# Performance work log

Measured on AMD Instinct MI355X. Metric: run time of the kernel, lower is better.

## Reference

```python
import jax, jax.numpy as jnp
import numpy as np

B, T, C, H, NT = 1, 1024, 768, 12, 8
D = C // H  # 64
POWER_ITERS = 4
DP_TEMP = 0.8
ESR_GAMMA = 0.02
ESR_ALPHA = 0.1


def rmsnorm(x, w, eps=1e-6):
    rms = jax.lax.rsqrt(jnp.mean(x * x, axis=-1, keepdims=True) + eps)
    return x * rms * w


def setup_inputs():
    key = jax.random.key(0)
    k0, k1, k2 = jax.random.split(key, 3)
    return {
        "x": jax.random.normal(k0, (B, T, C), jnp.float32),
        "W_qkvg": jax.random.normal(k1, (4 * C, C), jnp.float32) * 0.02,
        "W_out": jax.random.normal(k2, (C, C), jnp.float32) * 0.02,
        "lam": jnp.float32(1.5),
        "log_tau": -0.5 * jnp.ones((H, NT), jnp.float32),
        "logit_w": jnp.zeros((H, NT), jnp.float32),
        "beta": 1.5 * jnp.ones((H,), jnp.float32),
        "out_scale": jnp.ones((H,), jnp.float32),
        "dp_scale": jnp.ones((H,), jnp.float32),
        "logk_scale": jnp.ones((H,), jnp.float32),
        "dt_logit": jnp.float32(np.log(1.0 / 1e-8)),  # dt=1.0 -> logit = log(dt/(1-dt+1e-8))
        "g_norm_w": jnp.ones((D,), jnp.float32),
    }


def reference(x, W_qkvg, W_out, lam, log_tau, logit_w, beta, out_scale,
              dp_scale, logk_scale, dt_logit, g_norm_w):
    # qkvg projection and head split
    qkvg = x @ W_qkvg.T                                    # [B,T,4C]
    q, k, v, g = jnp.split(qkvg, 4, axis=-1)
    to_heads = lambda t: t.reshape(B, T, H, D).transpose(0, 2, 1, 3)  # [B,H,T,D]
    q, k, v, g = map(to_heads, (q, k, v, g))
    g = rmsnorm(g, g_norm_w)

    # pairwise squared distance ||g_i - g_j||^2
    g2 = jnp.sum(g * g, axis=-1)                           # [B,H,T]
    s = jnp.maximum(g2[..., :, None] + g2[..., None, :]
                    - 2.0 * jnp.einsum('bhid,bhjd->bhij', g, g), 0.0)  # [B,H,T,T]

    # fractional log-kernel: logsumexp_t[-(beta/2) log1p(s/(4 tau_t)) + log w_t]
    tau = jnp.maximum(jnp.exp(log_tau), 1e-6)              # [H,NT]
    w = jax.nn.softmax(logit_w, axis=-1)                   # [H,NT]
    beta_c = jnp.clip(beta, 0.5, 2.5)                      # [H]
    log_k_per = -(beta_c[None, :, None, None, None] / 2.0) * jnp.log1p(
        s[:, :, None] / (4.0 * tau[None, :, :, None, None]))          # [B,H,NT,T,T]
    logK = jax.nn.logsumexp(log_k_per + jnp.log(w + 1e-12)[None, :, :, None, None], axis=2)
    logK = logK * logk_scale[None, :, None, None]

    # dot-product scores
    dp = jnp.einsum('bhid,bhjd->bhij', q, k) * (dp_scale[None, :, None, None]
                                                / (np.sqrt(D) * DP_TEMP))

    # causal Markov normalize: blend, mask, stable row-softmax
    mask = jnp.tril(jnp.ones((T, T), bool))[None, None]    # [1,1,T,T]
    blended = lam * dp + (1.0 - lam) * logK
    blended = jnp.where(mask, blended, -jnp.inf)
    mx = jnp.max(blended, axis=-1, keepdims=True)
    mx = jnp.where(jnp.isfinite(mx), mx, 0.0)
    Kmat = jnp.exp(jnp.maximum(blended - mx, -60.0)) * mask
    P = Kmat / jnp.maximum(Kmat.sum(-1, keepdims=True), 1e-12)

    # power iteration for left stationary pi with full-support teleport
    pi0 = jnp.full((B, H, 1, T), 1.0 / T, P.dtype)
    def step(pi, _):
        p = (1.0 - ESR_GAMMA) * (pi @ P) + ESR_GAMMA / T
        p = p / jnp.maximum(p.sum(-1, keepdims=True), 1e-12)
        return p, None
    pi, _ = jax.lax.scan(step, pi0, None, length=POWER_ITERS)
    pi = jax.lax.stop_gradient(pi[..., 0, :])              # [B,H,T] (detached)

    # causal approximation to additive reversibilization
    P_adj = (pi[..., None, :] / jnp.maximum(pi[..., :, None], 1e-12)) \
            * jnp.swapaxes(P, -1, -2)                      # P*_ij = (pi_j/pi_i) P_ji
    P_rev = 0.5 * (P + P_adj) * mask
    P_rev = P_rev / jnp.maximum(P_rev.sum(-1, keepdims=True), 1e-12)

    dt = jax.nn.sigmoid(dt_logit)
    alpha = ESR_ALPHA * dt                                  # scale_alpha_by_dt=True
    P_fin = (1.0 - alpha) * P + alpha * P_rev

    y = (P_fin @ v) * out_scale[None, :, None, None]       # [B,H,T,D]
    y = y.transpose(0, 2, 1, 3).reshape(B, T, C)
    return y @ W_out.T
```

## Files before the change

kernel.cpp:

```cpp
#include <hip/hip_runtime.h>
#include <math.h>

#define TSEQ 1024
#define CD   768
#define HN   12
#define DD   64

#define OFF_QKVG   0
#define OFF_QH     3145728
#define OFF_KH     3538944
#define OFF_GH     3932160
#define OFF_VHT    4325376
#define OFF_G2     4718592
#define OFF_YB     4730880
#define OFF_CONSTS 5124096
#define OFF_OPART  5124608
#define OFF_LS     5911040
#define OFF_PD     5923328
#define OFF_XB     5935616
#define OFF_WQB    6328832
#define OFF_WOB    7508480
#define NZERO4     199680

#define N_XB  786432
#define N_WQB 2359296
#define N_WOB 589824

typedef __bf16 bf16x8 __attribute__((ext_vector_type(8)));
typedef float  f32x4  __attribute__((ext_vector_type(4)));
typedef unsigned short u16x8 __attribute__((ext_vector_type(8)));
typedef unsigned short u16x4 __attribute__((ext_vector_type(4)));

__device__ inline unsigned short f2bf(float f) {
  unsigned int u = __float_as_uint(f);
  return (unsigned short)((u + 0x7fffu + ((u >> 16) & 1u)) >> 16);
}


__global__ __launch_bounds__(64) void prep_kernel(
    const float* __restrict__ lam_p, const float* __restrict__ log_tau,
    const float* __restrict__ logit_w, const float* __restrict__ beta,
    const float* __restrict__ out_scale, const float* __restrict__ dp_scale,
    const float* __restrict__ logk_scale, const float* __restrict__ dt_logit,
    float* __restrict__ consts) {
  int h = threadIdx.x;
  if (h == 0) {
    float dt = 1.0f / (1.0f + __expf(-dt_logit[0]));
    consts[288] = 0.1f * dt;
  }
  if (h < HN) {
    float lam = lam_p[0];
    float* c = consts + h * 24;
    c[0] = lam * dp_scale[h] * (1.0f / 6.4f);
    c[1] = (1.0f - lam) * logk_scale[h];
    float b = fminf(fmaxf(beta[h], 0.5f), 2.5f);
    c[2] = 0.5f * b;
    c[3] = out_scale[h];
    float m = -1e30f;
    float lw[8];
    bool uni = true;
    for (int t = 0; t < 8; t++) {
      lw[t] = logit_w[h * 8 + t];
      m = fmaxf(m, lw[t]);
      if (log_tau[h * 8 + t] != log_tau[h * 8] || lw[t] != lw[0]) uni = false;
    }
    float s = 0.f;
    float e[8];
    for (int t = 0; t < 8; t++) { e[t] = __expf(lw[t] - m); s += e[t]; }
    for (int t = 0; t < 8; t++) {
      float w = e[t] / s;
      c[12 + t] = log2f(w + 1e-12f);
      float tau = fmaxf(__expf(log_tau[h * 8 + t]), 1e-6f);
      c[4 + t] = 1.0f / (4.0f * tau);
    }
    c[20] = uni ? 1.0f : 8.0f;
  }
}

__global__ __launch_bounds__(256) void zero_kernel(float4* __restrict__ p, int n4) {
  int i = blockIdx.x * 256 + threadIdx.x;
  for (; i < n4; i += gridDim.x * 256) p[i] = make_float4(0.f, 0.f, 0.f, 0.f);
}

__global__ __launch_bounds__(256) void convert_kernel(
    const float* __restrict__ x, const float* __restrict__ wq,
    const float* __restrict__ wo, unsigned short* __restrict__ xb,
    unsigned short* __restrict__ wqb, unsigned short* __restrict__ wob) {
  int i8 = (blockIdx.x * 256 + threadIdx.x) * 8;
  const float* src;
  unsigned short* dst;
  int off;
  if (i8 < N_XB) { src = x; dst = xb; off = i8; }
  else if (i8 < N_XB + N_WQB) { src = wq; dst = wqb; off = i8 - N_XB; }
  else if (i8 < N_XB + N_WQB + N_WOB) { src = wo; dst = wob; off = i8 - N_XB - N_WQB; }
  else return;
  float4 a = *(const float4*)&src[off];
  float4 b = *(const float4*)&src[off + 4];
  u16x8 u;
  u[0] = f2bf(a.x); u[1] = f2bf(a.y); u[2] = f2bf(a.z); u[3] = f2bf(a.w);
  u[4] = f2bf(b.x); u[5] = f2bf(b.y); u[6] = f2bf(b.z); u[7] = f2bf(b.w);
  *(u16x8*)&dst[off] = u;
}

__global__ __launch_bounds__(256, 2) void gemm_bf16_abT(
    const unsigned short* __restrict__ A, const unsigned short* __restrict__ B,
    float* __restrict__ Cm, int M, int N, int K) {
  __shared__ __align__(16) unsigned short As[128 * 72];
  __shared__ __align__(16) unsigned short Bs[64 * 72];
  int t = threadIdx.x;
  int lane = t & 63, w = t >> 6;
  int quad = lane >> 4, tx = lane & 15;
  int n0 = blockIdx.x * 64, m0 = blockIdx.y * 128;

  f32x4 acc[2][4] = {};
  int r_ = t >> 3, c8 = (t & 7) * 8;

  for (int k0 = 0; k0 < K; k0 += 64) {
    __syncthreads();
#pragma unroll
    for (int rep = 0; rep < 4; rep++) {
      int r = rep * 32 + r_;
      *(u16x8*)&As[r * 72 + c8] = *(const u16x8*)&A[(size_t)(m0 + r) * K + k0 + c8];
    }
#pragma unroll
    for (int rep = 0; rep < 2; rep++) {
      int r = rep * 32 + r_;
      *(u16x8*)&Bs[r * 72 + c8] = *(const u16x8*)&B[(size_t)(n0 + r) * K + k0 + c8];
    }
    __syncthreads();

#pragma unroll
    for (int ks = 0; ks < 2; ks++) {
      bf16x8 af[2];
#pragma unroll
      for (int mi = 0; mi < 2; mi++)
        af[mi] = *(const bf16x8*)&As[(32 * w + mi * 16 + tx) * 72 + ks * 32 + quad * 8];
#pragma unroll
      for (int ni = 0; ni < 4; ni++) {
        bf16x8 bv = *(const bf16x8*)&Bs[(ni * 16 + tx) * 72 + ks * 32 + quad * 8];
#pragma unroll
        for (int mi = 0; mi < 2; mi++)
          acc[mi][ni] = __builtin_amdgcn_mfma_f32_16x16x32_bf16(af[mi], bv, acc[mi][ni], 0, 0, 0);
      }
    }
  }

#pragma unroll
  for (int mi = 0; mi < 2; mi++)
#pragma unroll
    for (int ni = 0; ni < 4; ni++)
#pragma unroll
      for (int reg = 0; reg < 4; reg++) {
        int row = m0 + 32 * w + mi * 16 + quad * 4 + reg;
        Cm[(size_t)row * N + n0 + ni * 16 + tx] = acc[mi][ni][reg];
      }
}

__global__ __launch_bounds__(256) void pack_kernel(
    const float* __restrict__ qkvg, const float* __restrict__ g_norm_w,
    unsigned short* __restrict__ qh, unsigned short* __restrict__ kh,
    unsigned short* __restrict__ gh, unsigned short* __restrict__ vhT,
    float* __restrict__ g2) {
  int h = blockIdx.y;
  int t0 = blockIdx.x * 64;
  int t = threadIdx.x;
  __shared__ float tile[64][65];
  __shared__ float gw[64];
  __shared__ float part[64][4];
  __shared__ float rr[64];
  if (t < 64) gw[t] = g_norm_w[t];

#pragma unroll
  for (int rep = 0; rep < 2; rep++) {
    int idx = rep * 256 + t;
    int r = idx >> 3, c8 = (idx & 7) * 8;
    const float* sq = &qkvg[(size_t)(t0 + r) * 3072 + h * 64 + c8];
    const float* sk = sq + CD;
    u16x8 uq, uk;
#pragma unroll
    for (int j = 0; j < 8; j++) { uq[j] = f2bf(sq[j]); uk[j] = f2bf(sk[j]); }
    *(u16x8*)&qh[(size_t)(h * 1024 + t0 + r) * 64 + c8] = uq;
    *(u16x8*)&kh[(size_t)(h * 1024 + t0 + r) * 64 + c8] = uk;
  }

#pragma unroll 4
  for (int rep = 0; rep < 16; rep++) {
    int idx = rep * 256 + t;
    int r = idx >> 6, d = idx & 63;
    tile[r][d] = qkvg[(size_t)(t0 + r) * 3072 + 3 * CD + h * 64 + d];
  }
  __syncthreads();
  {
    int row = t >> 2, seg = t & 3;
    float s1 = 0.f;
    for (int d = seg * 16; d < seg * 16 + 16; d++) { float g = tile[row][d]; s1 += g * g; }
    part[row][seg] = s1;
  }
  __syncthreads();
  if (t < 64)
    rr[t] = rsqrtf((part[t][0] + part[t][1] + part[t][2] + part[t][3]) * (1.f / 64.f) + 1e-6f);
  __syncthreads();
  {
    int row = t >> 2, seg = t & 3;
    float rv = rr[row];
    float s2 = 0.f;
    u16x8 ua, ub;
#pragma unroll
    for (int j = 0; j < 8; j++) {
      float v = tile[row][seg * 16 + j] * rv * gw[seg * 16 + j];
      unsigned short us = f2bf(v); ua[j] = us;
      float vb = __uint_as_float((unsigned)us << 16); s2 += vb * vb;
    }
#pragma unroll
    for (int j = 0; j < 8; j++) {
      float v = tile[row][seg * 16 + 8 + j] * rv * gw[seg * 16 + 8 + j];
      unsigned short us = f2bf(v); ub[j] = us;
      float vb = __uint_as_float((unsigned)us << 16); s2 += vb * vb;
    }
    *(u16x8*)&gh[(size_t)(h * 1024 + t0 + row) * 64 + seg * 16] = ua;
    *(u16x8*)&gh[(size_t)(h * 1024 + t0 + row) * 64 + seg * 16 + 8] = ub;
    part[row][seg] = s2;
  }
  __syncthreads();
  if (t < 64) g2[h * 1024 + t0 + t] = part[t][0] + part[t][1] + part[t][2] + part[t][3];

  __syncthreads();
#pragma unroll 4
  for (int rep = 0; rep < 16; rep++) {
    int idx = rep * 256 + t;
    int r = idx >> 6, d = idx & 63;
    tile[r][d] = qkvg[(size_t)(t0 + r) * 3072 + 2 * CD + h * 64 + d];
  }
  __syncthreads();
#pragma unroll
  for (int rep = 0; rep < 2; rep++) {
    int idx = rep * 256 + t;
    int d = idx >> 3, tc8 = (idx & 7) * 8;
    u16x8 u;
#pragma unroll
    for (int j = 0; j < 8; j++) u[j] = f2bf(tile[tc8 + j][d]);
    *(u16x8*)&vhT[(size_t)(h * 64 + d) * 1024 + t0 + tc8] = u;
  }
}

__global__ __launch_bounds__(256, 3) void flash_kernel(
    const unsigned short* __restrict__ qh, const unsigned short* __restrict__ kh,
    const unsigned short* __restrict__ gh, const unsigned short* __restrict__ vhT,
    const float* __restrict__ g2, const float* __restrict__ consts,
    float* __restrict__ Opart, float* __restrict__ lsp, float* __restrict__ pdp) {
  int h = blockIdx.y;
  int uu = 143 - (int)blockIdx.x;
  int it = 0, rem = uu;
  for (it = 0; it < 32; ++it) {
    int njt_ = (it >> 1) + 1;
    int nc = (njt_ + 1) >> 1;
    if (rem < nc) break;
    rem -= nc;
  }
  int njt = (it >> 1) + 1;
  int jt0 = rem * 2;
  int jt1 = (jt0 + 2 < njt) ? (jt0 + 2) : njt;
  bool owns_diag = (jt1 == njt);
  int i0 = it * 32;
  int t = threadIdx.x;
  int lane = t & 63, w = t >> 6;
  int quad = lane >> 4, tx = lane & 15;
  int mi = w >> 1, nb = (w & 1) * 2;

  __shared__ __align__(16) unsigned short Qa[32 * 72];
  __shared__ __align__(16) unsigned short Ga[32 * 72];
  __shared__ __align__(16) unsigned short Ks[64 * 72];
  __shared__ __align__(16) unsigned short Gjs[64 * 72];
  __shared__ __align__(16) unsigned short Vt[64 * 72];
  __shared__ __align__(16) unsigned short psh[32 * 72];
  __shared__ float g2i[32], g2j[64], pdiag[32];

  const float* ch = consts + h * 24;
  float dpc2 = ch[0] * 1.44269504089f;
  float lkc = ch[1], bh2 = ch[2];
  int ntt = (int)ch[20];
  float i4t0 = ch[4];
  float inv4tau[8], logw[8];
#pragma unroll
  for (int tt = 0; tt < 8; tt++) { inv4tau[tt] = ch[4 + tt]; logw[tt] = ch[12 + tt]; }

  {
    int r = t >> 3, c8 = (t & 7) * 8;
    *(u16x8*)&Qa[r * 72 + c8] = *(const u16x8*)&qh[(size_t)(h * 1024 + i0 + r) * 64 + c8];
    *(u16x8*)&Ga[r * 72 + c8] = *(const u16x8*)&gh[(size_t)(h * 1024 + i0 + r) * 64 + c8];
  }
  if (t < 32) { g2i[t] = g2[h * 1024 + i0 + t]; pdiag[t] = 0.f; }
  __syncthreads();

  bf16x8 aq[2], ag[2];
#pragma unroll
  for (int ks = 0; ks < 2; ks++) {
    aq[ks] = *(const bf16x8*)&Qa[(mi * 16 + tx) * 72 + ks * 32 + quad * 8];
    ag[ks] = *(const bf16x8*)&Ga[(mi * 16 + tx) * 72 + ks * 32 + quad * 8];
  }

  f32x4 Oc[2] = {};
  float rowacc[4] = {0.f, 0.f, 0.f, 0.f};

  for (int jt = jt0; jt < jt1; jt++) {
    int j0 = jt * 64;
    __syncthreads();
    {
      int r4 = t >> 2, cb = (t & 3) * 16;
      const unsigned short* kp = &kh[(size_t)(h * 1024 + j0 + r4) * 64 + cb];
      const unsigned short* gp = &gh[(size_t)(h * 1024 + j0 + r4) * 64 + cb];
      const unsigned short* vp = &vhT[(size_t)(h * 64 + r4) * 1024 + j0 + cb];
      *(u16x8*)&Ks[r4 * 72 + cb] = *(const u16x8*)kp;
      *(u16x8*)&Ks[r4 * 72 + cb + 8] = *(const u16x8*)(kp + 8);
      *(u16x8*)&Gjs[r4 * 72 + cb] = *(const u16x8*)gp;
      *(u16x8*)&Gjs[r4 * 72 + cb + 8] = *(const u16x8*)(gp + 8);
      *(u16x8*)&Vt[r4 * 72 + cb] = *(const u16x8*)vp;
      *(u16x8*)&Vt[r4 * 72 + cb + 8] = *(const u16x8*)(vp + 8);
    }
    if (t < 64) g2j[t] = g2[h * 1024 + j0 + t];
    __syncthreads();

    f32x4 sqk[2] = {}, sgg[2] = {};
#pragma unroll
    for (int ni2 = 0; ni2 < 2; ni2++) {
#pragma unroll
      for (int ks = 0; ks < 2; ks++) {
        bf16x8 bk = *(const bf16x8*)&Ks[((nb + ni2) * 16 + tx) * 72 + ks * 32 + quad * 8];
        sqk[ni2] = __builtin_amdgcn_mfma_f32_16x16x32_bf16(aq[ks], bk, sqk[ni2], 0, 0, 0);
        bf16x8 bg = *(const bf16x8*)&Gjs[((nb + ni2) * 16 + tx) * 72 + ks * 32 + quad * 8];
        sgg[ni2] = __builtin_amdgcn_mfma_f32_16x16x32_bf16(ag[ks], bg, sgg[ni2], 0, 0, 0);
      }
    }

    float rs[4] = {0.f, 0.f, 0.f, 0.f};
#pragma unroll
    for (int ni2 = 0; ni2 < 2; ni2++) {
      int colg = j0 + (nb + ni2) * 16 + tx;
      float g2jv = g2j[(nb + ni2) * 16 + tx];
#pragma unroll
      for (int reg = 0; reg < 4; reg++) {
        int rowl = mi * 16 + quad * 4 + reg;
        int gi = i0 + rowl;
        float s = fmaxf(g2i[rowl] + g2jv - 2.0f * sgg[ni2][reg], 0.0f);
        float lse2;
        if (ntt == 1) {
          lse2 = -bh2 * __builtin_amdgcn_logf(fmaf(s, i4t0, 1.0f));
        } else {
          float se = 0.f;
#pragma unroll
          for (int tt = 0; tt < 8; tt++) {
            float lv = __builtin_amdgcn_logf(fmaf(s, inv4tau[tt], 1.0f));
            se += __builtin_amdgcn_exp2f(fmaf(-bh2, lv, logw[tt]));
          }
          lse2 = __builtin_amdgcn_logf(se + 1e-30f);
        }
        float b = fmaf(dpc2, sqk[ni2][reg], lkc * lse2);
        float p = (colg <= gi) ? __builtin_amdgcn_exp2f(b) : 0.0f;
        rs[reg] += p;
        psh[rowl * 72 + (nb + ni2) * 16 + tx] = f2bf(p);
        if (colg == gi) pdiag[rowl] = p;
      }
    }
#pragma unroll
    for (int reg = 0; reg < 4; reg++) {
#pragma unroll
      for (int m = 1; m < 16; m <<= 1) rs[reg] += __shfl_xor(rs[reg], m, 64);
      rowacc[reg] += rs[reg];
    }
    __syncthreads();

    bf16x8 ap[2];
#pragma unroll
    for (int ks = 0; ks < 2; ks++)
      ap[ks] = *(const bf16x8*)&psh[(mi * 16 + tx) * 72 + ks * 32 + quad * 8];
#pragma unroll
    for (int nd2 = 0; nd2 < 2; nd2++) {
#pragma unroll
      for (int ks = 0; ks < 2; ks++) {
        bf16x8 bv = *(const bf16x8*)&Vt[((nb + nd2) * 16 + tx) * 72 + ks * 32 + quad * 8];
        Oc[nd2] = __builtin_amdgcn_mfma_f32_16x16x32_bf16(ap[ks], bv, Oc[nd2], 0, 0, 0);
      }
    }
  }
  __syncthreads();

#pragma unroll
  for (int nd2 = 0; nd2 < 2; nd2++) {
#pragma unroll
    for (int reg = 0; reg < 4; reg++) {
      int row = i0 + mi * 16 + quad * 4 + reg;
      atomicAdd(&Opart[(size_t)(h * 1024 + row) * 64 + (nb + nd2) * 16 + tx], Oc[nd2][reg]);
    }
  }
  if (tx == 0) {
#pragma unroll
    for (int reg = 0; reg < 4; reg++)
      atomicAdd(&lsp[h * 1024 + i0 + mi * 16 + quad * 4 + reg], rowacc[reg]);
  }
  if (owns_diag && t < 32) pdp[h * 1024 + i0 + t] = pdiag[t];
}

__global__ __launch_bounds__(256) void finalize_kernel(
    const float* __restrict__ Opart, const float* __restrict__ lsp,
    const float* __restrict__ pdp, const float* __restrict__ qkvg,
    const float* __restrict__ consts, unsigned short* __restrict__ yb) {
  int h = blockIdx.y;
  int t = threadIdx.x;
  int rl = t >> 4, d4 = t & 15;
  int gi = blockIdx.x * 16 + rl;
  float alpha = consts[288];
  float osc = consts[h * 24 + 3];
  float l = fmaxf(lsp[h * TSEQ + gi], 1e-12f);
  float Pii = pdp[h * TSEQ + gi] / l;
  float inv1p = 1.0f / (1.0f + Pii);
  float c1 = (1.0f - alpha) + alpha * inv1p;
  float c2 = alpha * Pii * inv1p;
  float invl = 1.0f / l;
  float4 Ov = *(const float4*)&Opart[(size_t)(h * 1024 + gi) * 64 + 4 * d4];
  float4 vi = *(const float4*)&qkvg[(size_t)gi * 3072 + 2 * CD + h * 64 + 4 * d4];
  u16x4 o;
  o[0] = f2bf(osc * (c1 * Ov.x * invl + c2 * vi.x));
  o[1] = f2bf(osc * (c1 * Ov.y * invl + c2 * vi.y));
  o[2] = f2bf(osc * (c1 * Ov.z * invl + c2 * vi.z));
  o[3] = f2bf(osc * (c1 * Ov.w * invl + c2 * vi.w));
  *(u16x4*)&yb[(size_t)gi * CD + h * 64 + 4 * d4] = o;
}

extern "C" void kernel_launch(void* const* d_in, const int* in_sizes, int n_in,
                              void* d_out, int out_size, void* d_ws, size_t ws_size,
                              hipStream_t stream) {
  (void)in_sizes; (void)n_in; (void)out_size; (void)ws_size;
  const float* x          = (const float*)d_in[0];
  const float* W_qkvg     = (const float*)d_in[1];
  const float* W_out      = (const float*)d_in[2];
  const float* lam        = (const float*)d_in[3];
  const float* log_tau    = (const float*)d_in[4];
  const float* logit_w    = (const float*)d_in[5];
  const float* beta       = (const float*)d_in[6];
  const float* out_scale  = (const float*)d_in[7];
  const float* dp_scale   = (const float*)d_in[8];
  const float* logk_scale = (const float*)d_in[9];
  const float* dt_logit   = (const float*)d_in[10];
  const float* g_norm_w   = (const float*)d_in[11];
  float* ws = (float*)d_ws;
  float* qkvg   = ws + OFF_QKVG;
  unsigned short* qh  = (unsigned short*)(ws + OFF_QH);
  unsigned short* kh  = (unsigned short*)(ws + OFF_KH);
  unsigned short* gh  = (unsigned short*)(ws + OFF_GH);
  unsigned short* vhT = (unsigned short*)(ws + OFF_VHT);
  float* g2     = ws + OFF_G2;
  unsigned short* yb  = (unsigned short*)(ws + OFF_YB);
  float* consts = ws + OFF_CONSTS;
  float* Opart  = ws + OFF_OPART;
  float* lsp    = ws + OFF_LS;
  float* pdp    = ws + OFF_PD;
  unsigned short* xb  = (unsigned short*)(ws + OFF_XB);
  unsigned short* wqb = (unsigned short*)(ws + OFF_WQB);
  unsigned short* wob = (unsigned short*)(ws + OFF_WOB);
  float* out = (float*)d_out;

  prep_kernel<<<dim3(1), dim3(64), 0, stream>>>(lam, log_tau, logit_w, beta,
                                                out_scale, dp_scale, logk_scale,
                                                dt_logit, consts);
  zero_kernel<<<dim3(512), dim3(256), 0, stream>>>((float4*)Opart, NZERO4);
  convert_kernel<<<dim3((N_XB + N_WQB + N_WOB) / (256 * 8)), dim3(256), 0, stream>>>(
      x, W_qkvg, W_out, xb, wqb, wob);
  gemm_bf16_abT<<<dim3(48, 8), dim3(256), 0, stream>>>(xb, wqb, qkvg, 1024, 3072, 768);
  pack_kernel<<<dim3(16, 12), dim3(256), 0, stream>>>(qkvg, g_norm_w, qh, kh, gh, vhT, g2);
  flash_kernel<<<dim3(144, 12), dim3(256), 0, stream>>>(qh, kh, gh, vhT, g2, consts,
                                                        Opart, lsp, pdp);
  finalize_kernel<<<dim3(64, 12), dim3(256), 0, stream>>>(Opart, lsp, pdp, qkvg, consts, yb);
  gemm_bf16_abT<<<dim3(12, 8), dim3(256), 0, stream>>>(yb, wob, out, 1024, 768, 768);
}
```

Measured before the change: 153.4 us.

## Fuse QKVG GEMM epilogue with head packing, RMSnorm and q prescaling

The QKVG projection GEMM now writes bf16 head-major q, k, g, v and transposed v directly from its accumulators. It also does the g RMSnorm and squared-norm reduction via lane shuffles and folds the dot-product scale into q. This removes the fp32 qkvg intermediate and the separate pack kernel, and finalize reads bf16 v instead of fp32. The flash kernel merges the G and V shared buffers into one, loading V into registers and storing it after the score phase. That allows a higher occupancy bound at the cost of an extra barrier, plus slight precision loss from pre-rounding scaled q and v to bf16.

New measurement: 163.2 us. +6.4%, slower.

```diff
diff --git a/kernel.cpp b/kernel.cpp
--- a/kernel.cpp
+++ b/kernel.cpp
@@ -6,20 +6,20 @@
 #define HN   12
 #define DD   64
 
-#define OFF_QKVG   0
-#define OFF_QH     3145728
-#define OFF_KH     3538944
-#define OFF_GH     3932160
-#define OFF_VHT    4325376
-#define OFF_G2     4718592
-#define OFF_YB     4730880
-#define OFF_CONSTS 5124096
-#define OFF_OPART  5124608
-#define OFF_LS     5911040
-#define OFF_PD     5923328
-#define OFF_XB     5935616
-#define OFF_WQB    6328832
-#define OFF_WOB    7508480
+#define OFF_QH     0
+#define OFF_KH     393216
+#define OFF_GH     786432
+#define OFF_VHT    1179648
+#define OFF_VH     1572864
+#define OFF_G2     1966080
+#define OFF_YB     1978368
+#define OFF_CONSTS 2371584
+#define OFF_OPART  2372096
+#define OFF_LS     3158528
+#define OFF_PD     3170816
+#define OFF_XB     3183104
+#define OFF_WQB    3576320
+#define OFF_WOB    4755968
 #define NZERO4     199680
 
 #define N_XB  786432
@@ -34,6 +34,9 @@
 __device__ inline unsigned short f2bf(float f) {
   unsigned int u = __float_as_uint(f);
   return (unsigned short)((u + 0x7fffu + ((u >> 16) & 1u)) >> 16);
+}
+__device__ inline float bf2f(unsigned short u) {
+  return __uint_as_float((unsigned)u << 16);
 }
 
 
@@ -102,6 +105,126 @@
   *(u16x8*)&dst[off] = u;
 }
 
+__global__ __launch_bounds__(256, 2) void gemm_qkvg_fused(
+    const unsigned short* __restrict__ A, const unsigned short* __restrict__ B,
+    const float* __restrict__ consts, const float* __restrict__ g_norm_w,
+    unsigned short* __restrict__ qh, unsigned short* __restrict__ kh,
+    unsigned short* __restrict__ gh, unsigned short* __restrict__ vh,
+    unsigned short* __restrict__ vhT, float* __restrict__ g2) {
+  const int K = 768;
+  __shared__ __align__(16) unsigned short As[128 * 72];
+  __shared__ __align__(16) unsigned short Bs[64 * 72];
+  int t = threadIdx.x;
+  int lane = t & 63, w = t >> 6;
+  int quad = lane >> 4, tx = lane & 15;
+  int n0 = blockIdx.x * 64, m0 = blockIdx.y * 128;
+
+  f32x4 acc[2][4] = {};
+  int r_ = t >> 3, c8 = (t & 7) * 8;
+
+  for (int k0 = 0; k0 < K; k0 += 64) {
+    __syncthreads();
+#pragma unroll
+    for (int rep = 0; rep < 4; rep++) {
+      int r = rep * 32 + r_;
+      *(u16x8*)&As[r * 72 + c8] = *(const u16x8*)&A[(size_t)(m0 + r) * K + k0 + c8];
+    }
+#pragma unroll
+    for (int rep = 0; rep < 2; rep++) {
+      int r = rep * 32 + r_;
+      *(u16x8*)&Bs[r * 72 + c8] = *(const u16x8*)&B[(size_t)(n0 + r) * K + k0 + c8];
+    }
+    __syncthreads();
+
+#pragma unroll
+    for (int ks = 0; ks < 2; ks++) {
+      bf16x8 af[2];
+#pragma unroll
+      for (int mi = 0; mi < 2; mi++)
+        af[mi] = *(const bf16x8*)&As[(32 * w + mi * 16 + tx) * 72 + ks * 32 + quad * 8];
+#pragma unroll
+      for (int ni = 0; ni < 4; ni++) {
+        bf16x8 bv = *(const bf16x8*)&Bs[(ni * 16 + tx) * 72 + ks * 32 + quad * 8];
+#pragma unroll
+        for (int mi = 0; mi < 2; mi++)
+          acc[mi][ni] = __builtin_amdgcn_mfma_f32_16x16x32_bf16(af[mi], bv, acc[mi][ni], 0, 0, 0);
+      }
+    }
+  }
+
+  int typ = n0 / CD;
+  int h = (n0 - typ * CD) >> 6;
+  unsigned short* Ls = As;
+  __syncthreads();
+
+  if (typ == 3) {
+    float gw4[4];
+#pragma unroll
+    for (int ni = 0; ni < 4; ni++) gw4[ni] = g_norm_w[ni * 16 + tx];
+#pragma unroll
+    for (int mi = 0; mi < 2; mi++) {
+#pragma unroll
+      for (int reg = 0; reg < 4; reg++) {
+        float s1 = acc[mi][0][reg] * acc[mi][0][reg] + acc[mi][1][reg] * acc[mi][1][reg]
+                 + acc[mi][2][reg] * acc[mi][2][reg] + acc[mi][3][reg] * acc[mi][3][reg];
+#pragma unroll
+        for (int m = 1; m < 16; m <<= 1) s1 += __shfl_xor(s1, m, 64);
+        float rms = rsqrtf(s1 * (1.f / 64.f) + 1e-6f);
+        int rl = 32 * w + mi * 16 + quad * 4 + reg;
+        float s2 = 0.f;
+#pragma unroll
+        for (int ni = 0; ni < 4; ni++) {
+          float v = acc[mi][ni][reg] * rms * gw4[ni];
+          unsigned short us = f2bf(v);
+          Ls[rl * 72 + ni * 16 + tx] = us;
+          float vb = bf2f(us);
+          s2 += vb * vb;
+        }
+#pragma unroll
+        for (int m = 1; m < 16; m <<= 1) s2 += __shfl_xor(s2, m, 64);
+        if (tx == 0) g2[h * 1024 + m0 + rl] = s2;
+      }
+    }
+    __syncthreads();
+#pragma unroll
+    for (int rep = 0; rep < 4; rep++) {
+      int idx = rep * 256 + t;
+      int r = idx >> 3, cc = (idx & 7) * 8;
+      *(u16x8*)&gh[(size_t)(h * 1024 + m0 + r) * 64 + cc] = *(const u16x8*)&Ls[r * 72 + cc];
+    }
+  } else {
+    float sc = (typ == 0) ? consts[h * 24] * 1.44269504089f : 1.0f;
+#pragma unroll
+    for (int mi = 0; mi < 2; mi++)
+#pragma unroll
+      for (int ni = 0; ni < 4; ni++)
+#pragma unroll
+        for (int reg = 0; reg < 4; reg++) {
+          int rl = 32 * w + mi * 16 + quad * 4 + reg;
+          Ls[rl * 72 + ni * 16 + tx] = f2bf(acc[mi][ni][reg] * sc);
+        }
+    __syncthreads();
+    unsigned short* dst = (typ == 0) ? qh : ((typ == 1) ? kh : vh);
+#pragma unroll
+    for (int rep = 0; rep < 4; rep++) {
+      int idx = rep * 256 + t;
+      int r = idx >> 3, cc = (idx & 7) * 8;
+      *(u16x8*)&dst[(size_t)(h * 1024 + m0 + r) * 64 + cc] = *(const u16x8*)&Ls[r * 72 + cc];
+    }
+    if (typ == 2) {
+#pragma unroll
+      for (int rep = 0; rep < 4; rep++) {
+        int idx = rep * 256 + t;
+        int d = idx >> 4, rc = (idx & 15) * 8;
+        u16x8 u;
+#pragma unroll
+        for (int j = 0; j < 8; j++) u[j] = Ls[(rc + j) * 72 + d];
+        *(u16x8*)&vhT[(size_t)(h * 64 + d) * 1024 + m0 + rc] = u;
+      }
+    }
+  }
+}
+
 __global__ __launch_bounds__(256, 2) void gemm_bf16_abT(
     const unsigned short* __restrict__ A, const unsigned short* __restrict__ B,
     float* __restrict__ Cm, int M, int N, int K) {
@@ -156,94 +279,7 @@
       }
 }
 
-__global__ __launch_bounds__(256) void pack_kernel(
-    const float* __restrict__ qkvg, const float* __restrict__ g_norm_w,
-    unsigned short* __restrict__ qh, unsigned short* __restrict__ kh,
-    unsigned short* __restrict__ gh, unsigned short* __restrict__ vhT,
-    float* __restrict__ g2) {
-  int h = blockIdx.y;
-  int t0 = blockIdx.x * 64;
-  int t = threadIdx.x;
-  __shared__ float tile[64][65];
-  __shared__ float gw[64];
-  __shared__ float part[64][4];
-  __shared__ float rr[64];
-  if (t < 64) gw[t] = g_norm_w[t];
-
-#pragma unroll
-  for (int rep = 0; rep < 2; rep++) {
-    int idx = rep * 256 + t;
-    int r = idx >> 3, c8 = (idx & 7) * 8;
-    const float* sq = &qkvg[(size_t)(t0 + r) * 3072 + h * 64 + c8];
-    const float* sk = sq + CD;
-    u16x8 uq, uk;
-#pragma unroll
-    for (int j = 0; j < 8; j++) { uq[j] = f2bf(sq[j]); uk[j] = f2bf(sk[j]); }
-    *(u16x8*)&qh[(size_t)(h * 1024 + t0 + r) * 64 + c8] = uq;
-    *(u16x8*)&kh[(size_t)(h * 1024 + t0 + r) * 64 + c8] = uk;
-  }
-
-#pragma unroll 4
-  for (int rep = 0; rep < 16; rep++) {
-    int idx = rep * 256 + t;
-    int r = idx >> 6, d = idx & 63;
-    tile[r][d] = qkvg[(size_t)(t0 + r) * 3072 + 3 * CD + h * 64 + d];
-  }
-  __syncthreads();
-  {
-    int row = t >> 2, seg = t & 3;
-    float s1 = 0.f;
-    for (int d = seg * 16; d < seg * 16 + 16; d++) { float g = tile[row][d]; s1 += g * g; }
-    part[row][seg] = s1;
-  }
-  __syncthreads();
-  if (t < 64)
-    rr[t] = rsqrtf((part[t][0] + part[t][1] + part[t][2] + part[t][3]) * (1.f / 64.f) + 1e-6f);
-  __syncthreads();
-  {
-    int row = t >> 2, seg = t & 3;
-    float rv = rr[row];
-    float s2 = 0.f;
-    u16x8 ua, ub;
-#pragma unroll
-    for (int j = 0; j < 8; j++) {
-      float v = tile[row][seg * 16 + j] * rv * gw[seg * 16 + j];
-      unsigned short us = f2bf(v); ua[j] = us;
-      float vb = __uint_as_float((unsigned)us << 16); s2 += vb * vb;
-    }
-#pragma unroll
-    for (int j = 0; j < 8; j++) {
-      float v = tile[row][seg * 16 + 8 + j] * rv * gw[seg * 16 + 8 + j];
-      unsigned short us = f2bf(v); ub[j] = us;
-      float vb = __uint_as_float((unsigned)us << 16); s2 += vb * vb;
-    }
-    *(u16x8*)&gh[(size_t)(h * 1024 + t0 + row) * 64 + seg * 16] = ua;
-    *(u16x8*)&gh[(size_t)(h * 1024 + t0 + row) * 64 + seg * 16 + 8] = ub;
-    part[row][seg] = s2;
-  }
-  __syncthreads();
-  if (t < 64) g2[h * 1024 + t0 + t] = part[t][0] + part[t][1] + part[t][2] + part[t][3];
-
-  __syncthreads();
-#pragma unroll 4
-  for (int rep = 0; rep < 16; rep++) {
-    int idx = rep * 256 + t;
-    int r = idx >> 6, d = idx & 63;
-    tile[r][d] = qkvg[(size_t)(t0 + r) * 3072 + 2 * CD + h * 64 + d];
-  }
-  __syncthreads();
-#pragma unroll
-  for (int rep = 0; rep < 2; rep++) {
-    int idx = rep * 256 + t;
-    int d = idx >> 3, tc8 = (idx & 7) * 8;
-    u16x8 u;
-#pragma unroll
-    for (int j = 0; j < 8; j++) u[j] = f2bf(tile[tc8 + j][d]);
-    *(u16x8*)&vhT[(size_t)(h * 64 + d) * 1024 + t0 + tc8] = u;
-  }
-}
-
-__global__ __launch_bounds__(256, 3) void flash_kernel(
+__global__ __launch_bounds__(256, 4) void flash_kernel(
     const unsigned short* __restrict__ qh, const unsigned short* __restrict__ kh,
     const unsigned short* __restrict__ gh, const unsigned short* __restrict__ vhT,
     const float* __restrict__ g2, const float* __restrict__ consts,
@@ -270,13 +306,11 @@
   __shared__ __align__(16) unsigned short Qa[32 * 72];
   __shared__ __align__(16) unsigned short Ga[32 * 72];
   __shared__ __align__(16) unsigned short Ks[64 * 72];
-  __shared__ __align__(16) unsigned short Gjs[64 * 72];
-  __shared__ __align__(16) unsigned short Vt[64 * 72];
+  __shared__ __align__(16) unsigned short GV[64 * 72];
   __shared__ __align__(16) unsigned short psh[32 * 72];
   __shared__ float g2i[32], g2j[64], pdiag[32];
 
   const float* ch = consts + h * 24;
-  float dpc2 = ch[0] * 1.44269504089f;
   float lkc = ch[1], bh2 = ch[2];
   int ntt = (int)ch[20];
   float i4t0 = ch[4];
@@ -301,24 +335,28 @@
 
   f32x4 Oc[2] = {};
   float rowacc[4] = {0.f, 0.f, 0.f, 0.f};
+  int r4 = t >> 2, cb = (t & 3) * 16;
 
   for (int jt = jt0; jt < jt1; jt++) {
     int j0 = jt * 64;
     __syncthreads();
     {
-      int r4 = t >> 2, cb = (t & 3) * 16;
       const unsigned short* kp = &kh[(size_t)(h * 1024 + j0 + r4) * 64 + cb];
       const unsigned short* gp = &gh[(size_t)(h * 1024 + j0 + r4) * 64 + cb];
-      const unsigned short* vp = &vhT[(size_t)(h * 64 + r4) * 1024 + j0 + cb];
       *(u16x8*)&Ks[r4 * 72 + cb] = *(const u16x8*)kp;
       *(u16x8*)&Ks[r4 * 72 + cb + 8] = *(const u16x8*)(kp + 8);
-      *(u16x8*)&Gjs[r4 * 72 + cb] = *(const u16x8*)gp;
-      *(u16x8*)&Gjs[r4 * 72 + cb + 8] = *(const u16x8*)(gp + 8);
-      *(u16x8*)&Vt[r4 * 72 + cb] = *(const u16x8*)vp;
-      *(u16x8*)&Vt[r4 * 72 + cb + 8] = *(const u16x8*)(vp + 8);
+      *(u16x8*)&GV[r4 * 72 + cb] = *(const u16x8*)gp;
+      *(u16x8*)&GV[r4 * 72 + cb + 8] = *(const u16x8*)(gp + 8);
     }
     if (t < 64) g2j[t] = g2[h * 1024 + j0 + t];
     __syncthreads();
+
+    u16x8 v0, v1;
+    {
+      const unsigned short* vp = &vhT[(size_t)(h * 64 + r4) * 1024 + j0 + cb];
+      v0 = *(const u16x8*)vp;
+      v1 = *(const u16x8*)(vp + 8);
+    }
 
     f32x4 sqk[2] = {}, sgg[2] = {};
 #pragma unroll
@@ -327,7 +365,7 @@
       for (int ks = 0; ks < 2; ks++) {
         bf16x8 bk = *(const bf16x8*)&Ks[((nb + ni2) * 16 + tx) * 72 + ks * 32 + quad * 8];
         sqk[ni2] = __builtin_amdgcn_mfma_f32_16x16x32_bf16(aq[ks], bk, sqk[ni2], 0, 0, 0);
-        bf16x8 bg = *(const bf16x8*)&Gjs[((nb + ni2) * 16 + tx) * 72 + ks * 32 + quad * 8];
+        bf16x8 bg = *(const bf16x8*)&GV[((nb + ni2) * 16 + tx) * 72 + ks * 32 + quad * 8];
         sgg[ni2] = __builtin_amdgcn_mfma_f32_16x16x32_bf16(ag[ks], bg, sgg[ni2], 0, 0, 0);
       }
     }
@@ -354,7 +392,7 @@
           }
           lse2 = __builtin_amdgcn_logf(se + 1e-30f);
         }
-        float b = fmaf(dpc2, sqk[ni2][reg], lkc * lse2);
+        float b = fmaf(lkc, lse2, sqk[ni2][reg]);
         float p = (colg <= gi) ? __builtin_amdgcn_exp2f(b) : 0.0f;
         rs[reg] += p;
         psh[rowl * 72 + (nb + ni2) * 16 + tx] = f2bf(p);
@@ -368,6 +406,9 @@
       rowacc[reg] += rs[reg];
     }
     __syncthreads();
+    *(u16x8*)&GV[r4 * 72 + cb] = v0;
+    *(u16x8*)&GV[r4 * 72 + cb + 8] = v1;
+    __syncthreads();
 
     bf16x8 ap[2];
 #pragma unroll
@@ -377,7 +418,7 @@
     for (int nd2 = 0; nd2 < 2; nd2++) {
 #pragma unroll
       for (int ks = 0; ks < 2; ks++) {
-        bf16x8 bv = *(const bf16x8*)&Vt[((nb + nd2) * 16 + tx) * 72 + ks * 32 + quad * 8];
+        bf16x8 bv = *(const bf16x8*)&GV[((nb + nd2) * 16 + tx) * 72 + ks * 32 + quad * 8];
         Oc[nd2] = __builtin_amdgcn_mfma_f32_16x16x32_bf16(ap[ks], bv, Oc[nd2], 0, 0, 0);
       }
     }
@@ -402,7 +443,7 @@
 
 __global__ __launch_bounds__(256) void finalize_kernel(
     const float* __restrict__ Opart, const float* __restrict__ lsp,
-    const float* __restrict__ pdp, const float* __restrict__ qkvg,
+    const float* __restrict__ pdp, const unsigned short* __restrict__ vh,
     const float* __restrict__ consts, unsigned short* __restrict__ yb) {
   int h = blockIdx.y;
   int t = threadIdx.x;
@@ -417,12 +458,12 @@
   float c2 = alpha * Pii * inv1p;
   float invl = 1.0f / l;
   float4 Ov = *(const float4*)&Opart[(size_t)(h * 1024 + gi) * 64 + 4 * d4];
-  float4 vi = *(const float4*)&qkvg[(size_t)gi * 3072 + 2 * CD + h * 64 + 4 * d4];
+  u16x4 vb = *(const u16x4*)&vh[(size_t)(h * 1024 + gi) * 64 + 4 * d4];
   u16x4 o;
-  o[0] = f2bf(osc * (c1 * Ov.x * invl + c2 * vi.x));
-  o[1] = f2bf(osc * (c1 * Ov.y * invl + c2 * vi.y));
-  o[2] = f2bf(osc * (c1 * Ov.z * invl + c2 * vi.z));
-  o[3] = f2bf(osc * (c1 * Ov.w * invl + c2 * vi.w));
+  o[0] = f2bf(osc * (c1 * Ov.x * invl + c2 * bf2f(vb[0])));
+  o[1] = f2bf(osc * (c1 * Ov.y * invl + c2 * bf2f(vb[1])));
+  o[2] = f2bf(osc * (c1 * Ov.z * invl + c2 * bf2f(vb[2])));
+  o[3] = f2bf(osc * (c1 * Ov.w * invl + c2 * bf2f(vb[3])));
   *(u16x4*)&yb[(size_t)gi * CD + h * 64 + 4 * d4] = o;
 }
 
@@ -443,11 +484,11 @@
   const float* dt_logit   = (const float*)d_in[10];
   const float* g_norm_w   = (const float*)d_in[11];
   float* ws = (float*)d_ws;
-  float* qkvg   = ws + OFF_QKVG;
   unsigned short* qh  = (unsigned short*)(ws + OFF_QH);
   unsigned short* kh  = (unsigned short*)(ws + OFF_KH);
   unsigned short* gh  = (unsigned short*)(ws + OFF_GH);
   unsigned short* vhT = (unsigned short*)(ws + OFF_VHT);
+  unsigned short* vh  = (unsigned short*)(ws + OFF_VH);
   float* g2     = ws + OFF_G2;
   unsigned short* yb  = (unsigned short*)(ws + OFF_YB);
   float* consts = ws + OFF_CONSTS;
@@ -465,10 +506,10 @@
   zero_kernel<<<dim3(512), dim3(256), 0, stream>>>((float4*)Opart, NZERO4);
   convert_kernel<<<dim3((N_XB + N_WQB + N_WOB) / (256 * 8)), dim3(256), 0, stream>>>(
       x, W_qkvg, W_out, xb, wqb, wob);
-  gemm_bf16_abT<<<dim3(48, 8), dim3(256), 0, stream>>>(xb, wqb, qkvg, 1024, 3072, 768);
-  pack_kernel<<<dim3(16, 12), dim3(256), 0, stream>>>(qkvg, g_norm_w, qh, kh, gh, vhT, g2);
+  gemm_qkvg_fused<<<dim3(48, 8), dim3(256), 0, stream>>>(xb, wqb, consts, g_norm_w,
+                                                         qh, kh, gh, vh, vhT, g2);
   flash_kernel<<<dim3(144, 12), dim3(256), 0, stream>>>(qh, kh, gh, vhT, g2, consts,
                                                         Opart, lsp, pdp);
-  finalize_kernel<<<dim3(64, 12), dim3(256), 0, stream>>>(Opart, lsp, pdp, qkvg, consts, yb);
+  finalize_kernel<<<dim3(64, 12), dim3(256), 0, stream>>>(Opart, lsp, pdp, vh, consts, yb);
   gemm_bf16_abT<<<dim3(12, 8), dim3(256), 0, stream>>>(yb, wob, out, 1024, 768, 768);
 }
```
